# Kernel optimization log

Hardware: AMD Instinct MI355X
Metric: run time of the kernel (lower is better)

## Reference

```python
import jax, jax.numpy as jnp
import numpy as np

C, B, D, Fq, T, H = 4, 2, 128, 256, 256, 4


def setup_inputs() -> dict:
    key = jax.random.key(0)
    ks = jax.random.split(key, 8)
    s = 0.05
    return {
        "h_all": jax.random.normal(ks[0], (C, B, D, Fq, T), jnp.float32),
        "ln_q_g": jnp.ones((D,), jnp.float32),
        "ln_q_b": jnp.zeros((D,), jnp.float32),
        "ln_kv_g": jnp.ones((D,), jnp.float32),
        "ln_kv_b": jnp.zeros((D,), jnp.float32),
        "Wq": jax.random.normal(ks[1], (D, D), jnp.float32) * s,
        "bq": jnp.zeros((D,), jnp.float32),
        "Wk": jax.random.normal(ks[2], (D, D), jnp.float32) * s,
        "bk": jnp.zeros((D,), jnp.float32),
        "Wv": jax.random.normal(ks[3], (D, D), jnp.float32) * s,
        "bv": jnp.zeros((D,), jnp.float32),
        "in_w": jax.random.normal(ks[4], (3 * D, D), jnp.float32) * s,
        "in_b": jnp.zeros((3 * D,), jnp.float32),
        "out_w": jax.random.normal(ks[5], (D, D), jnp.float32) * s,
        "out_b": jnp.zeros((D,), jnp.float32),
    }


def _ln(x, g, b):
    # LayerNorm over last dim, eps=1e-5 (torch default, biased variance)
    m = jnp.mean(x, axis=-1, keepdims=True)
    v = jnp.var(x, axis=-1, keepdims=True)
    return (x - m) * jax.lax.rsqrt(v + 1e-5) * g + b


def reference(h_all, ln_q_g, ln_q_b, ln_kv_g, ln_kv_b, Wq, bq, Wk, bk, Wv, bv, in_w, in_b, out_w, out_b):
    c, b_, d, f, t = h_all.shape
    h = H
    hd = d // h
    n = b_ * f * t  # flattened batch B*F*T
    # (B,d,F,T) -> (N, d) reference sequence (seq len 1 squeezed)
    h_ref_seq = jnp.transpose(h_all[0], (0, 2, 3, 1)).reshape(n, d)
    # (C,B,d,F,T) -> (N, C, d)
    h_all_seq = jnp.transpose(h_all, (1, 3, 4, 0, 2)).reshape(n, c, d)
    # module's own projections
    Q = _ln(h_ref_seq, ln_q_g, ln_q_b) @ Wq.T + bq  # (N, d)
    kv_n = _ln(h_all_seq, ln_kv_g, ln_kv_b)         # (N, C, d)
    K = kv_n @ Wk.T + bk                            # (N, C, d)
    V = kv_n @ Wv.T + bv                            # (N, C, d)
    # nn.MultiheadAttention internal in_proj (packed q/k/v) + out_proj
    q = (Q @ in_w[:d].T + in_b[:d]).reshape(n, h, hd)                    # (N,H,hd)
    k = (K @ in_w[d:2 * d].T + in_b[d:2 * d]).reshape(n, c, h, hd)       # (N,C,H,hd)
    v = (V @ in_w[2 * d:].T + in_b[2 * d:]).reshape(n, c, h, hd)         # (N,C,H,hd)
    scores = jnp.einsum('nhd,nchd->nhc', q, k) / jnp.sqrt(jnp.float32(hd))
    attn = jax.nn.softmax(scores, axis=-1)
    ctx = jnp.einsum('nhc,nchd->nhd', attn, v).reshape(n, d)
    out = ctx @ out_w.T + out_b + h_ref_seq  # residual
    return jnp.transpose(out.reshape(b_, f, t, d), (0, 3, 1, 2))  # (B,d,F,T)
```

## Files before the change

### kernel.cpp

```cpp
#include <hip/hip_runtime.h>
#include <hip/hip_bf16.h>

typedef unsigned short u16;
typedef unsigned int   u32;

#define D_ 128
#define B_ 2
#define F_ 256
#define T_ 256
#define FT (F_*T_)
#define XS 136
#define QS 40

typedef __bf16 bf16x8 __attribute__((ext_vector_type(8)));
typedef float  floatx16 __attribute__((ext_vector_type(16)));

#define LGKM0 asm volatile("s_waitcnt lgkmcnt(0)" ::: "memory")

__device__ __forceinline__ u16 f2bf(float f) {
    union { __hip_bfloat16 h; u16 u; } cv; cv.h = __float2bfloat16(f); return cv.u;
}
__device__ __forceinline__ u32 pk2(float lo, float hi2) {
    union { __hip_bfloat162 h; u32 u; } cv;
    cv.h = __float22bfloat162_rn(make_float2(lo, hi2)); return cv.u;
}
__device__ __forceinline__ float bf2f(u16 u) { return __uint_as_float(((u32)u) << 16); }

__global__ __launch_bounds__(128) void precompute_eff(
    const float* __restrict__ lnqg, const float* __restrict__ lnqb,
    const float* __restrict__ lnkg, const float* __restrict__ lnkb,
    const float* __restrict__ Wq, const float* __restrict__ bq,
    const float* __restrict__ Wk, const float* __restrict__ bk,
    const float* __restrict__ Wv, const float* __restrict__ bv,
    const float* __restrict__ in_w, const float* __restrict__ in_b,
    const float* __restrict__ ow,
    u16* __restrict__ Agb, u16* __restrict__ Ob,
    float* __restrict__ sA, float* __restrict__ cb)
{
    const int j = blockIdx.x;
    const int sel = blockIdx.y;
    const int i = threadIdx.x;
    if (sel == 3) { Ob[j*D_ + i] = f2bf(ow[j*D_ + i]); return; }

    const float* W  = (sel==0) ? Wq : (sel==1) ? Wk : Wv;
    const float* bW = (sel==0) ? bq : (sel==1) ? bk : bv;
    const float* g  = (sel==0) ? lnqg : lnkg;
    const float* bl = (sel==0) ? lnqb : lnkb;

    __shared__ float row[D_];
    __shared__ float red[D_];
    row[i] = in_w[(sel*D_ + j)*D_ + i];
    __syncthreads();
    float acc = 0.f;
    #pragma unroll 8
    for (int m = 0; m < D_; ++m) acc = fmaf(row[m], W[m*D_ + i], acc);
    float ag = acc * g[i];
    Agb[sel*D_*D_ + j*D_ + i] = f2bf(ag);

    red[i] = ag;
    __syncthreads();
    for (int s = 64; s > 0; s >>= 1) { if (i < s) red[i] += red[i+s]; __syncthreads(); }
    if (i == 0) sA[sel*D_ + j] = red[0];
    __syncthreads();
    red[i] = acc * bl[i] + row[i] * bW[i];
    __syncthreads();
    for (int s = 64; s > 0; s >>= 1) { if (i < s) red[i] += red[i+s]; __syncthreads(); }
    if (i == 0) cb[sel*D_ + j] = red[0] + in_b[sel*D_ + j];
}

__global__ __launch_bounds__(256, 3) void cca_mfma(
    const float* __restrict__ h,
    const u16*  __restrict__ Agb,
    const u16*  __restrict__ Ob,
    const float* __restrict__ sA,
    const float* __restrict__ cbp,
    const float* __restrict__ out_b,
    float* __restrict__ outp)
{
    __shared__ __align__(16) u16 xb[4][32*XS];
    __shared__ __align__(16) u16 qk[4][32*QS];
    __shared__ float swt[4][4][32];
    __shared__ float rmneg[4][32];
    __shared__ float invr[32];

    const int tid = threadIdx.x;
    const int blk = blockIdx.x;
    const int t0 = (blk & 7) * 32;
    const int f  = (blk >> 3) & 255;
    const int b  = blk >> 11;

    {
        const int dd = tid >> 3;
        const int t4 = (tid & 7) * 4;
        #pragma unroll
        for (int it = 0; it < 2; ++it) {
            const int d = 2*dd + 64*it;
            #pragma unroll
            for (int c = 0; c < 4; ++c) {
                const float* p = h + ((size_t)((c*B_ + b)*D_ + d))*FT + (size_t)f*T_ + t0 + t4;
                float4 v0 = *(const float4*)p;
                float4 v1 = *(const float4*)(p + FT);
                u32* dst = (u32*)xb[c] + dd + 32*it;
                dst[(size_t)(t4+0)*(XS/2)] = pk2(v0.x, v1.x);
                dst[(size_t)(t4+1)*(XS/2)] = pk2(v0.y, v1.y);
                dst[(size_t)(t4+2)*(XS/2)] = pk2(v0.z, v1.z);
                dst[(size_t)(t4+3)*(XS/2)] = pk2(v0.w, v1.w);
            }
        }
    }
    __syncthreads();

    {
        const int rowi = tid >> 1, half = tid & 1;
        const int c = rowi >> 5, t = rowi & 31;
        u32* rowp = (u32*)(xb[c] + t*XS) + half*32;
        u32 rw[32];
        #pragma unroll
        for (int i = 0; i < 8; ++i) {
            uint4 q = ((const uint4*)rowp)[i];
            rw[4*i] = q.x; rw[4*i+1] = q.y; rw[4*i+2] = q.z; rw[4*i+3] = q.w;
        }
        float s = 0.f, sq = 0.f;
        #pragma unroll
        for (int k = 0; k < 32; ++k) {
            float lo = __uint_as_float(rw[k] << 16);
            float hi2 = __uint_as_float(rw[k] & 0xffff0000u);
            s += lo + hi2;
            sq = fmaf(lo, lo, fmaf(hi2, hi2, sq));
        }
        s += __shfl_xor(s, 1);
        sq += __shfl_xor(sq, 1);
        float m = s * (1.f/128.f);
        float var = fmaf(-m, m, sq * (1.f/128.f));
        float r = rsqrtf(var + 1e-5f);
        #pragma unroll
        for (int i = 0; i < 8; ++i) {
            uint4 q;
            q.x = pk2(__uint_as_float(rw[4*i]   << 16)*r, __uint_as_float(rw[4*i]   & 0xffff0000u)*r);
            q.y = pk2(__uint_as_float(rw[4*i+1] << 16)*r, __uint_as_float(rw[4*i+1] & 0xffff0000u)*r);
            q.z = pk2(__uint_as_float(rw[4*i+2] << 16)*r, __uint_as_float(rw[4*i+2] & 0xffff0000u)*r);
            q.w = pk2(__uint_as_float(rw[4*i+3] << 16)*r, __uint_as_float(rw[4*i+3] & 0xffff0000u)*r);
            ((uint4*)rowp)[i] = q;
        }
        if (half == 0) {
            rmneg[c][t] = -r*m;
            if (c == 0) invr[t] = 1.0f / r;
        }
    }
    __syncthreads();

    const int wv  = tid >> 6;
    const int l   = tid & 63;
    const int lo5 = l & 31, hi = l >> 5;
    const int jq  = wv*32 + lo5;
    u16* qkw = qk[wv];
    const int xoff  = lo5*XS + hi*8;
    const int qkoff = lo5*QS + hi*8;

    const u16* Bq = Agb +         (size_t)jq*D_ + hi*8;
    const u16* Bk = Agb + 16384 + (size_t)jq*D_ + hi*8;
    const u16* Bv = Agb + 32768 + (size_t)jq*D_ + hi*8;
    const u16* Bo = Ob  +         (size_t)jq*D_ + hi*8;
    const float sAq = sA[jq],      cbq = cbp[jq];
    const float sAk = sA[128+jq],  cbk = cbp[128+jq];
    const float sAv = sA[256+jq],  cbv = cbp[256+jq];

    auto foldv = [&](floatx16& a, int c, float sAx, float cbx) {
        #pragma unroll
        for (int g = 0; g < 4; ++g) {
            float4 rm4 = *(const float4*)&rmneg[c][8*g + 4*hi];
            a[4*g+0] += fmaf(rm4.x, sAx, cbx);
            a[4*g+1] += fmaf(rm4.y, sAx, cbx);
            a[4*g+2] += fmaf(rm4.z, sAx, cbx);
            a[4*g+3] += fmaf(rm4.w, sAx, cbx);
        }
    };
    auto stage = [&](const floatx16& a) {
        #pragma unroll
        for (int i = 0; i < 16; ++i) {
            const int t = (i&3) + 8*(i>>2) + 4*hi;
            qkw[t*QS + lo5] = f2bf(a[i]);
        }
    };
    auto diag = [&](const floatx16& s2) -> float {
        const bool b0 = lo5 & 1, b1 = lo5 & 2, b2 = lo5 & 8, b3 = lo5 & 16;
        float t01 = b0 ? s2[1] : s2[0],  t23 = b0 ? s2[3] : s2[2];
        float t45 = b0 ? s2[5] : s2[4],  t67 = b0 ? s2[7] : s2[6];
        float t89 = b0 ? s2[9] : s2[8],  tab = b0 ? s2[11] : s2[10];
        float tcd = b0 ? s2[13] : s2[12], tef = b0 ? s2[15] : s2[14];
        float u0 = b1 ? t23 : t01, u1 = b1 ? t67 : t45;
        float u2 = b1 ? tab : t89, u3 = b1 ? tef : tcd;
        float v0 = b2 ? u1 : u0,  v1 = b2 ? u3 : u2;
        return b3 ? v1 : v0;
    };

    floatx16 qa;
    #pragma unroll
    for (int i = 0; i < 16; ++i) qa[i] = 0.f;
    __builtin_amdgcn_s_setprio(1);
    #pragma unroll
    for (int ks = 0; ks < 8; ++ks) {
        bf16x8 a  = *(const bf16x8*)(xb[0] + xoff + ks*16);
        bf16x8 bb = *(const bf16x8*)(Bq + ks*16);
        qa = __builtin_amdgcn_mfma_f32_32x32x16_bf16(a, bb, qa, 0, 0, 0);
    }
    __builtin_amdgcn_s_setprio(0);
    foldv(qa, 0, sAq, cbq);
    stage(qa);
    LGKM0;
    bf16x8 qf0 = *(const bf16x8*)(qkw + qkoff);
    bf16x8 qf1 = *(const bf16x8*)(qkw + qkoff + 16);
    LGKM0;

    floatx16 ka0, ka1, ka2, ka3;
    #pragma unroll
    for (int i = 0; i < 16; ++i) { ka0[i]=0.f; ka1[i]=0.f; ka2[i]=0.f; ka3[i]=0.f; }
    __builtin_amdgcn_s_setprio(1);
    #pragma unroll
    for (int ks = 0; ks < 8; ++ks) {
        bf16x8 bb = *(const bf16x8*)(Bk + ks*16);
        bf16x8 a0 = *(const bf16x8*)(xb[0] + xoff + ks*16);
        bf16x8 a1 = *(const bf16x8*)(xb[1] + xoff + ks*16);
        bf16x8 a2 = *(const bf16x8*)(xb[2] + xoff + ks*16);
        bf16x8 a3 = *(const bf16x8*)(xb[3] + xoff + ks*16);
        ka0 = __builtin_amdgcn_mfma_f32_32x32x16_bf16(a0, bb, ka0, 0, 0, 0);
        ka1 = __builtin_amdgcn_mfma_f32_32x32x16_bf16(a1, bb, ka1, 0, 0, 0);
        ka2 = __builtin_amdgcn_mfma_f32_32x32x16_bf16(a2, bb, ka2, 0, 0, 0);
        ka3 = __builtin_amdgcn_mfma_f32_32x32x16_bf16(a3, bb, ka3, 0, 0, 0);
    }
    __builtin_amdgcn_s_setprio(0);
    float sreg[4];
    #pragma unroll
    for (int c = 0; c < 4; ++c) {
        floatx16& ka = (c==0) ? ka0 : (c==1) ? ka1 : (c==2) ? ka2 : ka3;
        foldv(ka, c, sAk, cbk);
        stage(ka);
        LGKM0;
        bf16x8 kf0 = *(const bf16x8*)(qkw + qkoff);
        bf16x8 kf1 = *(const bf16x8*)(qkw + qkoff + 16);
        LGKM0;
        floatx16 sc;
        #pragma unroll
        for (int i = 0; i < 16; ++i) sc[i] = 0.f;
        __builtin_amdgcn_s_setprio(1);
        sc = __builtin_amdgcn_mfma_f32_32x32x16_bf16(qf0, kf0, sc, 0, 0, 0);
        sc = __builtin_amdgcn_mfma_f32_32x32x16_bf16(qf1, kf1, sc, 0, 0, 0);
        __builtin_amdgcn_s_setprio(0);
        sreg[c] = diag(sc) * 0.17677669529663687f;
    }

    {
        const bool active = (hi == ((lo5 >> 2) & 1));
        if (active) {
            float mm = fmaxf(fmaxf(sreg[0], sreg[1]), fmaxf(sreg[2], sreg[3]));
            float e0 = __expf(sreg[0]-mm), e1 = __expf(sreg[1]-mm);
            float e2 = __expf(sreg[2]-mm), e3 = __expf(sreg[3]-mm);
            float inv = 1.f / (e0+e1+e2+e3);
            swt[wv][0][lo5] = e0*inv; swt[wv][1][lo5] = e1*inv;
            swt[wv][2][lo5] = e2*inv; swt[wv][3][lo5] = e3*inv;
        }
    }
    LGKM0;

    floatx16 ctx;
    #pragma unroll
    for (int i = 0; i < 16; ++i) ctx[i] = 0.f;
    #pragma unroll
    for (int cp = 0; cp < 4; cp += 2) {
        floatx16 va0, va1;
        #pragma unroll
        for (int i = 0; i < 16; ++i) { va0[i]=0.f; va1[i]=0.f; }
        __builtin_amdgcn_s_setprio(1);
        #pragma unroll
        for (int ks = 0; ks < 8; ++ks) {
            bf16x8 bb = *(const bf16x8*)(Bv + ks*16);
            bf16x8 a0 = *(const bf16x8*)(xb[cp]   + xoff + ks*16);
            bf16x8 a1 = *(const bf16x8*)(xb[cp+1] + xoff + ks*16);
            va0 = __builtin_amdgcn_mfma_f32_32x32x16_bf16(a0, bb, va0, 0, 0, 0);
            va1 = __builtin_amdgcn_mfma_f32_32x32x16_bf16(a1, bb, va1, 0, 0, 0);
        }
        __builtin_amdgcn_s_setprio(0);
        #pragma unroll
        for (int d = 0; d < 2; ++d) {
            const int c = cp + d;
            floatx16& va = d ? va1 : va0;
            foldv(va, c, sAv, cbv);
            #pragma unroll
            for (int g = 0; g < 4; ++g) {
                float4 w4 = *(const float4*)&swt[wv][c][8*g + 4*hi];
                ctx[4*g+0] = fmaf(w4.x, va[4*g+0], ctx[4*g+0]);
                ctx[4*g+1] = fmaf(w4.y, va[4*g+1], ctx[4*g+1]);
                ctx[4*g+2] = fmaf(w4.z, va[4*g+2], ctx[4*g+2]);
                ctx[4*g+3] = fmaf(w4.w, va[4*g+3], ctx[4*g+3]);
            }
        }
    }

    __syncthreads();
    #pragma unroll
    for (int i = 0; i < 16; ++i) {
        const int t = (i&3) + 8*(i>>2) + 4*hi;
        xb[1][t*XS + jq] = f2bf(ctx[i]);
    }
    __syncthreads();

    floatx16 oa;
    #pragma unroll
    for (int i = 0; i < 16; ++i) oa[i] = 0.f;
    __builtin_amdgcn_s_setprio(1);
    #pragma unroll
    for (int ks = 0; ks < 8; ++ks) {
        bf16x8 a  = *(const bf16x8*)(xb[1] + xoff + ks*16);
        bf16x8 bb = *(const bf16x8*)(Bo + ks*16);
        oa = __builtin_amdgcn_mfma_f32_32x32x16_bf16(a, bb, oa, 0, 0, 0);
    }
    __builtin_amdgcn_s_setprio(0);
    const float obv = out_b[jq];
    float* obase = outp + ((size_t)(b*D_ + jq))*FT + (size_t)f*T_ + t0;
    #pragma unroll
    for (int g = 0; g < 4; ++g) {
        const int tb = 8*g + 4*hi;
        float4 iv4 = *(const float4*)&invr[tb];
        float4 st;
        st.x = oa[g*4+0] + obv + bf2f(xb[0][(tb+0)*XS + jq]) * iv4.x;
        st.y = oa[g*4+1] + obv + bf2f(xb[0][(tb+1)*XS + jq]) * iv4.y;
        st.z = oa[g*4+2] + obv + bf2f(xb[0][(tb+2)*XS + jq]) * iv4.z;
        st.w = oa[g*4+3] + obv + bf2f(xb[0][(tb+3)*XS + jq]) * iv4.w;
        *(float4*)(obase + tb) = st;
    }
}

extern "C" void kernel_launch(void* const* d_in, const int* in_sizes, int n_in,
                              void* d_out, int out_size, void* d_ws, size_t ws_size,
                              hipStream_t stream) {
    const float* h    = (const float*)d_in[0];
    const float* lnqg = (const float*)d_in[1];
    const float* lnqb = (const float*)d_in[2];
    const float* lnkg = (const float*)d_in[3];
    const float* lnkb = (const float*)d_in[4];
    const float* Wq   = (const float*)d_in[5];
    const float* bq   = (const float*)d_in[6];
    const float* Wk   = (const float*)d_in[7];
    const float* bk   = (const float*)d_in[8];
    const float* Wv   = (const float*)d_in[9];
    const float* bv   = (const float*)d_in[10];
    const float* in_w = (const float*)d_in[11];
    const float* in_b = (const float*)d_in[12];
    const float* ow   = (const float*)d_in[13];
    const float* ob   = (const float*)d_in[14];

    char* ws = (char*)d_ws;
    u16*   Agb = (u16*)ws;
    u16*   Obf = (u16*)(ws + 98304);
    float* sAe = (float*)(ws + 98304 + 32768);
    float* cbe = (float*)(ws + 98304 + 32768 + 1536);

    precompute_eff<<<dim3(128, 4), 128, 0, stream>>>(
        lnqg, lnqb, lnkg, lnkb, Wq, bq, Wk, bk, Wv, bv,
        in_w, in_b, ow, Agb, Obf, sAe, cbe);
    cca_mfma<<<dim3(B_*F_*(T_/32)), 256, 0, stream>>>(
        h, Agb, Obf, sAe, cbe, ob, (float*)d_out);
}
```

Before: 483.6 us.

## Transpose MFMA operands so scores compute in registers without LDS staging

Swaps the A/B operands of the projection MFMAs so each lane holds a single token's features across its accumulator. Per-head q·k dot products then become a lane-local FMA reduction plus one cross-half shuffle, replacing the LDS round trip of q/k staging, the extra score MFMAs and the diagonal extraction. Softmax weights stay in registers and the ctx write-back is packed. The LDS buffers it frees allow occupancy to go from 3 to 4 blocks per CU, at the cost of more per-lane FMA work and per-element bias vectors held in registers.

```diff
diff --git a/kernel.cpp b/kernel.cpp
--- a/kernel.cpp
+++ b/kernel.cpp
@@ -10,12 +10,9 @@
 #define T_ 256
 #define FT (F_*T_)
 #define XS 136
-#define QS 40
 
 typedef __bf16 bf16x8 __attribute__((ext_vector_type(8)));
 typedef float  floatx16 __attribute__((ext_vector_type(16)));
-
-#define LGKM0 asm volatile("s_waitcnt lgkmcnt(0)" ::: "memory")
 
 __device__ __forceinline__ u16 f2bf(float f) {
     union { __hip_bfloat16 h; u16 u; } cv; cv.h = __float2bfloat16(f); return cv.u;
@@ -68,7 +65,7 @@
     if (i == 0) cb[sel*D_ + j] = red[0] + in_b[sel*D_ + j];
 }
 
-__global__ __launch_bounds__(256, 3) void cca_mfma(
+__global__ __launch_bounds__(256, 4) void cca_mfma(
     const float* __restrict__ h,
     const u16*  __restrict__ Agb,
     const u16*  __restrict__ Ob,
@@ -78,8 +75,6 @@
     float* __restrict__ outp)
 {
     __shared__ __align__(16) u16 xb[4][32*XS];
-    __shared__ __align__(16) u16 qk[4][32*QS];
-    __shared__ float swt[4][4][32];
     __shared__ float rmneg[4][32];
     __shared__ float invr[32];
 
@@ -153,45 +148,21 @@
     const int l   = tid & 63;
     const int lo5 = l & 31, hi = l >> 5;
     const int jq  = wv*32 + lo5;
-    u16* qkw = qk[wv];
-    const int xoff  = lo5*XS + hi*8;
-    const int qkoff = lo5*QS + hi*8;
+    const int xoff = lo5*XS + hi*8;
 
     const u16* Bq = Agb +         (size_t)jq*D_ + hi*8;
     const u16* Bk = Agb + 16384 + (size_t)jq*D_ + hi*8;
     const u16* Bv = Agb + 32768 + (size_t)jq*D_ + hi*8;
     const u16* Bo = Ob  +         (size_t)jq*D_ + hi*8;
-    const float sAq = sA[jq],      cbq = cbp[jq];
-    const float sAk = sA[128+jq],  cbk = cbp[128+jq];
-    const float sAv = sA[256+jq],  cbv = cbp[256+jq];
-
-    auto foldv = [&](floatx16& a, int c, float sAx, float cbx) {
+
+    auto ldvec = [&](const float* base) -> floatx16 {
+        floatx16 r;
         #pragma unroll
         for (int g = 0; g < 4; ++g) {
-            float4 rm4 = *(const float4*)&rmneg[c][8*g + 4*hi];
-            a[4*g+0] += fmaf(rm4.x, sAx, cbx);
-            a[4*g+1] += fmaf(rm4.y, sAx, cbx);
-            a[4*g+2] += fmaf(rm4.z, sAx, cbx);
-            a[4*g+3] += fmaf(rm4.w, sAx, cbx);
-        }
-    };
-    auto stage = [&](const floatx16& a) {
-        #pragma unroll
-        for (int i = 0; i < 16; ++i) {
-            const int t = (i&3) + 8*(i>>2) + 4*hi;
-            qkw[t*QS + lo5] = f2bf(a[i]);
-        }
-    };
-    auto diag = [&](const floatx16& s2) -> float {
-        const bool b0 = lo5 & 1, b1 = lo5 & 2, b2 = lo5 & 8, b3 = lo5 & 16;
-        float t01 = b0 ? s2[1] : s2[0],  t23 = b0 ? s2[3] : s2[2];
-        float t45 = b0 ? s2[5] : s2[4],  t67 = b0 ? s2[7] : s2[6];
-        float t89 = b0 ? s2[9] : s2[8],  tab = b0 ? s2[11] : s2[10];
-        float tcd = b0 ? s2[13] : s2[12], tef = b0 ? s2[15] : s2[14];
-        float u0 = b1 ? t23 : t01, u1 = b1 ? t67 : t45;
-        float u2 = b1 ? tab : t89, u3 = b1 ? tef : tcd;
-        float v0 = b2 ? u1 : u0,  v1 = b2 ? u3 : u2;
-        return b3 ? v1 : v0;
+            float4 v = *(const float4*)(base + wv*32 + 8*g + 4*hi);
+            r[4*g+0]=v.x; r[4*g+1]=v.y; r[4*g+2]=v.z; r[4*g+3]=v.w;
+        }
+        return r;
     };
 
     floatx16 qa;
@@ -200,107 +171,102 @@
     __builtin_amdgcn_s_setprio(1);
     #pragma unroll
     for (int ks = 0; ks < 8; ++ks) {
-        bf16x8 a  = *(const bf16x8*)(xb[0] + xoff + ks*16);
-        bf16x8 bb = *(const bf16x8*)(Bq + ks*16);
-        qa = __builtin_amdgcn_mfma_f32_32x32x16_bf16(a, bb, qa, 0, 0, 0);
+        bf16x8 w = *(const bf16x8*)(Bq + ks*16);
+        bf16x8 a = *(const bf16x8*)(xb[0] + xoff + ks*16);
+        qa = __builtin_amdgcn_mfma_f32_32x32x16_bf16(w, a, qa, 0, 0, 0);
     }
     __builtin_amdgcn_s_setprio(0);
-    foldv(qa, 0, sAq, cbq);
-    stage(qa);
-    LGKM0;
-    bf16x8 qf0 = *(const bf16x8*)(qkw + qkoff);
-    bf16x8 qf1 = *(const bf16x8*)(qkw + qkoff + 16);
-    LGKM0;
-
-    floatx16 ka0, ka1, ka2, ka3;
-    #pragma unroll
-    for (int i = 0; i < 16; ++i) { ka0[i]=0.f; ka1[i]=0.f; ka2[i]=0.f; ka3[i]=0.f; }
-    __builtin_amdgcn_s_setprio(1);
-    #pragma unroll
-    for (int ks = 0; ks < 8; ++ks) {
-        bf16x8 bb = *(const bf16x8*)(Bk + ks*16);
-        bf16x8 a0 = *(const bf16x8*)(xb[0] + xoff + ks*16);
-        bf16x8 a1 = *(const bf16x8*)(xb[1] + xoff + ks*16);
-        bf16x8 a2 = *(const bf16x8*)(xb[2] + xoff + ks*16);
-        bf16x8 a3 = *(const bf16x8*)(xb[3] + xoff + ks*16);
-        ka0 = __builtin_amdgcn_mfma_f32_32x32x16_bf16(a0, bb, ka0, 0, 0, 0);
-        ka1 = __builtin_amdgcn_mfma_f32_32x32x16_bf16(a1, bb, ka1, 0, 0, 0);
-        ka2 = __builtin_amdgcn_mfma_f32_32x32x16_bf16(a2, bb, ka2, 0, 0, 0);
-        ka3 = __builtin_amdgcn_mfma_f32_32x32x16_bf16(a3, bb, ka3, 0, 0, 0);
-    }
-    __builtin_amdgcn_s_setprio(0);
+    {
+        floatx16 sAq_ = ldvec(sA);
+        floatx16 cbq_ = ldvec(cbp);
+        const float rm = rmneg[0][lo5];
+        #pragma unroll
+        for (int i = 0; i < 16; ++i) qa[i] += fmaf(rm, sAq_[i], cbq_[i]);
+    }
+
     float sreg[4];
-    #pragma unroll
-    for (int c = 0; c < 4; ++c) {
-        floatx16& ka = (c==0) ? ka0 : (c==1) ? ka1 : (c==2) ? ka2 : ka3;
-        foldv(ka, c, sAk, cbk);
-        stage(ka);
-        LGKM0;
-        bf16x8 kf0 = *(const bf16x8*)(qkw + qkoff);
-        bf16x8 kf1 = *(const bf16x8*)(qkw + qkoff + 16);
-        LGKM0;
-        floatx16 sc;
-        #pragma unroll
-        for (int i = 0; i < 16; ++i) sc[i] = 0.f;
-        __builtin_amdgcn_s_setprio(1);
-        sc = __builtin_amdgcn_mfma_f32_32x32x16_bf16(qf0, kf0, sc, 0, 0, 0);
-        sc = __builtin_amdgcn_mfma_f32_32x32x16_bf16(qf1, kf1, sc, 0, 0, 0);
-        __builtin_amdgcn_s_setprio(0);
-        sreg[c] = diag(sc) * 0.17677669529663687f;
-    }
-
-    {
-        const bool active = (hi == ((lo5 >> 2) & 1));
-        if (active) {
-            float mm = fmaxf(fmaxf(sreg[0], sreg[1]), fmaxf(sreg[2], sreg[3]));
-            float e0 = __expf(sreg[0]-mm), e1 = __expf(sreg[1]-mm);
-            float e2 = __expf(sreg[2]-mm), e3 = __expf(sreg[3]-mm);
-            float inv = 1.f / (e0+e1+e2+e3);
-            swt[wv][0][lo5] = e0*inv; swt[wv][1][lo5] = e1*inv;
-            swt[wv][2][lo5] = e2*inv; swt[wv][3][lo5] = e3*inv;
-        }
-    }
-    LGKM0;
+    {
+        floatx16 sAk_ = ldvec(sA + 128);
+        floatx16 cbk_ = ldvec(cbp + 128);
+        #pragma unroll
+        for (int cp = 0; cp < 4; cp += 2) {
+            floatx16 k0, k1;
+            #pragma unroll
+            for (int i = 0; i < 16; ++i) { k0[i]=0.f; k1[i]=0.f; }
+            __builtin_amdgcn_s_setprio(1);
+            #pragma unroll
+            for (int ks = 0; ks < 8; ++ks) {
+                bf16x8 w  = *(const bf16x8*)(Bk + ks*16);
+                bf16x8 a0 = *(const bf16x8*)(xb[cp]   + xoff + ks*16);
+                bf16x8 a1 = *(const bf16x8*)(xb[cp+1] + xoff + ks*16);
+                k0 = __builtin_amdgcn_mfma_f32_32x32x16_bf16(w, a0, k0, 0, 0, 0);
+                k1 = __builtin_amdgcn_mfma_f32_32x32x16_bf16(w, a1, k1, 0, 0, 0);
+            }
+            __builtin_amdgcn_s_setprio(0);
+            const float rm0 = rmneg[cp][lo5], rm1 = rmneg[cp+1][lo5];
+            float p0 = 0.f, p1 = 0.f;
+            #pragma unroll
+            for (int i = 0; i < 16; ++i) {
+                p0 = fmaf(qa[i], k0[i] + fmaf(rm0, sAk_[i], cbk_[i]), p0);
+                p1 = fmaf(qa[i], k1[i] + fmaf(rm1, sAk_[i], cbk_[i]), p1);
+            }
+            p0 += __shfl_xor(p0, 32);
+            p1 += __shfl_xor(p1, 32);
+            sreg[cp]   = p0 * 0.17677669529663687f;
+            sreg[cp+1] = p1 * 0.17677669529663687f;
+        }
+    }
+
+    float w0, w1, w2, w3;
+    {
+        float mm = fmaxf(fmaxf(sreg[0], sreg[1]), fmaxf(sreg[2], sreg[3]));
+        float e0 = __expf(sreg[0]-mm), e1 = __expf(sreg[1]-mm);
+        float e2 = __expf(sreg[2]-mm), e3 = __expf(sreg[3]-mm);
+        float inv = 1.f / (e0+e1+e2+e3);
+        w0 = e0*inv; w1 = e1*inv; w2 = e2*inv; w3 = e3*inv;
+    }
 
     floatx16 ctx;
     #pragma unroll
     for (int i = 0; i < 16; ++i) ctx[i] = 0.f;
-    #pragma unroll
-    for (int cp = 0; cp < 4; cp += 2) {
-        floatx16 va0, va1;
-        #pragma unroll
-        for (int i = 0; i < 16; ++i) { va0[i]=0.f; va1[i]=0.f; }
-        __builtin_amdgcn_s_setprio(1);
-        #pragma unroll
-        for (int ks = 0; ks < 8; ++ks) {
-            bf16x8 bb = *(const bf16x8*)(Bv + ks*16);
-            bf16x8 a0 = *(const bf16x8*)(xb[cp]   + xoff + ks*16);
-            bf16x8 a1 = *(const bf16x8*)(xb[cp+1] + xoff + ks*16);
-            va0 = __builtin_amdgcn_mfma_f32_32x32x16_bf16(a0, bb, va0, 0, 0, 0);
-            va1 = __builtin_amdgcn_mfma_f32_32x32x16_bf16(a1, bb, va1, 0, 0, 0);
-        }
-        __builtin_amdgcn_s_setprio(0);
-        #pragma unroll
-        for (int d = 0; d < 2; ++d) {
-            const int c = cp + d;
-            floatx16& va = d ? va1 : va0;
-            foldv(va, c, sAv, cbv);
-            #pragma unroll
-            for (int g = 0; g < 4; ++g) {
-                float4 w4 = *(const float4*)&swt[wv][c][8*g + 4*hi];
-                ctx[4*g+0] = fmaf(w4.x, va[4*g+0], ctx[4*g+0]);
-                ctx[4*g+1] = fmaf(w4.y, va[4*g+1], ctx[4*g+1]);
-                ctx[4*g+2] = fmaf(w4.z, va[4*g+2], ctx[4*g+2]);
-                ctx[4*g+3] = fmaf(w4.w, va[4*g+3], ctx[4*g+3]);
-            }
-        }
-    }
-
-    __syncthreads();
-    #pragma unroll
-    for (int i = 0; i < 16; ++i) {
-        const int t = (i&3) + 8*(i>>2) + 4*hi;
-        xb[1][t*XS + jq] = f2bf(ctx[i]);
+    {
+        floatx16 sAv_ = ldvec(sA + 256);
+        floatx16 cbv_ = ldvec(cbp + 256);
+        #pragma unroll
+        for (int cp = 0; cp < 4; cp += 2) {
+            floatx16 va0, va1;
+            #pragma unroll
+            for (int i = 0; i < 16; ++i) { va0[i]=0.f; va1[i]=0.f; }
+            __builtin_amdgcn_s_setprio(1);
+            #pragma unroll
+            for (int ks = 0; ks < 8; ++ks) {
+                bf16x8 w  = *(const bf16x8*)(Bv + ks*16);
+                bf16x8 a0 = *(const bf16x8*)(xb[cp]   + xoff + ks*16);
+                bf16x8 a1 = *(const bf16x8*)(xb[cp+1] + xoff + ks*16);
+                va0 = __builtin_amdgcn_mfma_f32_32x32x16_bf16(w, a0, va0, 0, 0, 0);
+                va1 = __builtin_amdgcn_mfma_f32_32x32x16_bf16(w, a1, va1, 0, 0, 0);
+            }
+            __builtin_amdgcn_s_setprio(0);
+            #pragma unroll
+            for (int d = 0; d < 2; ++d) {
+                const int c = cp + d;
+                floatx16& va = d ? va1 : va0;
+                const float rm  = rmneg[c][lo5];
+                const float wgt = (c==0) ? w0 : (c==1) ? w1 : (c==2) ? w2 : w3;
+                #pragma unroll
+                for (int i = 0; i < 16; ++i)
+                    ctx[i] = fmaf(wgt, va[i] + fmaf(rm, sAv_[i], cbv_[i]), ctx[i]);
+            }
+        }
+    }
+
+    __syncthreads();
+    #pragma unroll
+    for (int g = 0; g < 4; ++g) {
+        uint2 wr;
+        wr.x = pk2(ctx[4*g+0], ctx[4*g+1]);
+        wr.y = pk2(ctx[4*g+2], ctx[4*g+3]);
+        *(uint2*)(xb[1] + lo5*XS + wv*32 + 8*g + 4*hi) = wr;
     }
     __syncthreads();
 
```

Result: slower. 528.8 us (+9.3%).
